# Optimization experiments

Hardware: AMD Instinct MI355X
Metric: run time of the kernel (lower is better)

Reference implementation:

```python
import jax, jax.numpy as jnp
import numpy as np

B, T, V, E, H = 256, 512, 30000, 256, 32


def _run_dir(x, mask, Wih, Whh, bih, bhh, reverse):
    # x: [B,T,D], mask: [B,T] bool. PyTorch GRU gate order: r, z, n.
    gi = jnp.einsum('btd,gd->btg', x, Wih) + bih  # precompute input gates [B,T,3H]
    h0 = jnp.zeros((x.shape[0], Whh.shape[1]), x.dtype)

    def step(h, inp):
        gi_t, m_t = inp
        gh = h @ Whh.T + bhh
        ir, iz, inn = jnp.split(gi_t, 3, axis=-1)
        hr, hz, hn = jnp.split(gh, 3, axis=-1)
        r = jax.nn.sigmoid(ir + hr)
        z = jax.nn.sigmoid(iz + hz)
        n = jnp.tanh(inn + r * hn)
        h_new = (1.0 - z) * n + z * h
        # packed-sequence semantics: freeze state at padded steps
        h = jnp.where(m_t[:, None], h_new, h)
        return h, h

    hT, ys = jax.lax.scan(step, h0, (jnp.swapaxes(gi, 0, 1), mask.T), reverse=reverse)
    return jnp.swapaxes(ys, 0, 1), hT  # outputs [B,T,H], final hidden [B,H]


def _bigru_layer(x, mask, pf, pb):
    of, hf = _run_dir(x, mask, *pf, reverse=False)
    ob, hb = _run_dir(x, mask, *pb, reverse=True)
    return jnp.concatenate([of, ob], axis=-1), hf, hb


def setup_inputs() -> dict:
    key = jax.random.key(0)
    ks = jax.random.split(key, 24)
    lengths = jax.random.randint(ks[0], (B,), 1, T + 1)
    mask = (jnp.arange(T)[None, :] < lengths[:, None]).astype(jnp.int32)
    ids = jax.random.randint(ks[1], (B, T), 1, V)
    ids = jnp.where(mask > 0, ids, 0)  # pad_id = 0 at padded positions
    embed = (jax.random.normal(ks[2], (V, E), jnp.float32) * 0.1).at[0].set(0.0)

    def gru_params(k, din):
        k1, k2, k3, k4 = jax.random.split(k, 4)
        s = 1.0 / np.sqrt(H)
        return (jax.random.uniform(k1, (3 * H, din), jnp.float32, -s, s),
                jax.random.uniform(k2, (3 * H, H), jnp.float32, -s, s),
                jax.random.uniform(k3, (3 * H,), jnp.float32, -s, s),
                jax.random.uniform(k4, (3 * H,), jnp.float32, -s, s))

    inp = {"input_ids": ids, "attention_mask": mask, "embed": embed}
    i = 3
    for layer, din in (("l0", E), ("l1", 2 * H)):
        for d in ("f", "b"):
            Wih, Whh, bih, bhh = gru_params(ks[i], din); i += 1
            inp[f"Wih_{layer}{d}"] = Wih
            inp[f"Whh_{layer}{d}"] = Whh
            inp[f"bih_{layer}{d}"] = bih
            inp[f"bhh_{layer}{d}"] = bhh
    s = 1.0 / np.sqrt(2 * H)
    inp["Wout"] = jax.random.uniform(ks[i], (6, 2 * H), jnp.float32, -s, s)
    inp["bout"] = jax.random.uniform(ks[i + 1], (6,), jnp.float32, -s, s)
    return inp


def reference(input_ids, attention_mask, embed,
              Wih_l0f, Whh_l0f, bih_l0f, bhh_l0f,
              Wih_l0b, Whh_l0b, bih_l0b, bhh_l0b,
              Wih_l1f, Whh_l1f, bih_l1f, bhh_l1f,
              Wih_l1b, Whh_l1b, bih_l1b, bhh_l1b,
              Wout, bout):
    mask = attention_mask > 0
    x = embed[input_ids]  # [B,T,E]
    x1, _, _ = _bigru_layer(x, mask,
                            (Wih_l0f, Whh_l0f, bih_l0f, bhh_l0f),
                            (Wih_l0b, Whh_l0b, bih_l0b, bhh_l0b))
    # no dropout: eval-mode forward
    _, hf, hb = _bigru_layer(x1, mask,
                             (Wih_l1f, Whh_l1f, bih_l1f, bhh_l1f),
                             (Wih_l1b, Whh_l1b, bih_l1b, bhh_l1b))
    top = jnp.concatenate([hf, hb], axis=-1)  # h_n[-2:] -> [B, 2H]
    return top @ Wout.T + bout  # [B, 6]
```

## Files before the change

kernel.cpp:

```cpp
#include <hip/hip_runtime.h>
#include <hip/hip_bf16.h>
#include <stdint.h>

#define B_ 256
#define T_ 512
#define V_ 30000
#define E_ 256
#define H_ 32

typedef float v2f __attribute__((ext_vector_type(2)));

__device__ __forceinline__ float sigmoidf_fast(float x) {
    return 1.0f / (1.0f + __expf(-x));
}
__device__ __forceinline__ float tanhf_fast(float x) {
    return 1.0f - 2.0f / (1.0f + __expf(2.0f * x));
}
__device__ __forceinline__ uint32_t rlu(float v, int lane) {
    return (uint32_t)__builtin_amdgcn_readlane(__float_as_int(v), lane);
}
__device__ __forceinline__ void pk_fma(v2f& acc, v2f w, uint64_t hh) {
    asm("v_pk_fma_f32 %0, %1, %2, %0" : "+v"(acc) : "v"(w), "s"(hh));
}

#define GEMM_MT 64
#define GEMM_KC 32
#define GEMM_PA 68
#define GEMM_PB 196

__global__ __launch_bounds__(256) void gemm_gates(
    const float* __restrict__ A, int M, int K,
    const float* __restrict__ Wf, const float* __restrict__ Wb,
    const float* __restrict__ bihf, const float* __restrict__ bhhf,
    const float* __restrict__ bihb, const float* __restrict__ bhhb,
    float* __restrict__ Out)
{
    __shared__ float As[GEMM_KC][GEMM_PA];
    __shared__ float Bs[GEMM_KC][GEMM_PB];

    const int tid = threadIdx.x;
    const int mbase = blockIdx.x * GEMM_MT;
    const int mg = tid >> 5, ng = tid & 31;
    const int m_off = mg * 8, n_off = ng * 6;

    float acc[8][6];
    #pragma unroll
    for (int r = 0; r < 8; ++r)
        #pragma unroll
        for (int c = 0; c < 6; ++c) acc[r][c] = 0.f;

    for (int kc = 0; kc < K; kc += GEMM_KC) {
        #pragma unroll
        for (int i = 0; i < 2; ++i) {
            int fi = tid + 256 * i;
            int row = fi >> 3, cf = fi & 7;
            int m = mbase + row;
            float4 v = make_float4(0.f, 0.f, 0.f, 0.f);
            if (m < M) v = *(const float4*)&A[(size_t)m * K + kc + cf * 4];
            As[cf * 4 + 0][row] = v.x; As[cf * 4 + 1][row] = v.y;
            As[cf * 4 + 2][row] = v.z; As[cf * 4 + 3][row] = v.w;
        }
        #pragma unroll
        for (int i = 0; i < 6; ++i) {
            int fi = tid + 256 * i;
            int g = fi >> 3, cf = fi & 7;
            const float* Wsel = (g < 96) ? (Wf + (size_t)g * K)
                                         : (Wb + (size_t)(g - 96) * K);
            float4 v = *(const float4*)&Wsel[kc + cf * 4];
            Bs[cf * 4 + 0][g] = v.x; Bs[cf * 4 + 1][g] = v.y;
            Bs[cf * 4 + 2][g] = v.z; Bs[cf * 4 + 3][g] = v.w;
        }
        __syncthreads();
        #pragma unroll
        for (int k = 0; k < GEMM_KC; ++k) {
            float a[8], bb[6];
            *(float4*)&a[0] = *(const float4*)&As[k][m_off];
            *(float4*)&a[4] = *(const float4*)&As[k][m_off + 4];
            *(float2*)&bb[0] = *(const float2*)&Bs[k][n_off];
            *(float2*)&bb[2] = *(const float2*)&Bs[k][n_off + 2];
            *(float2*)&bb[4] = *(const float2*)&Bs[k][n_off + 4];
            #pragma unroll
            for (int r = 0; r < 8; ++r)
                #pragma unroll
                for (int c = 0; c < 6; ++c)
                    acc[r][c] = fmaf(a[r], bb[c], acc[r][c]);
        }
        __syncthreads();
    }

    float bias[6];
    #pragma unroll
    for (int c = 0; c < 6; ++c) {
        int g = n_off + c;
        int g96 = (g < 96) ? g : g - 96;
        const float* bih = (g < 96) ? bihf : bihb;
        const float* bhh = (g < 96) ? bhhf : bhhb;
        bias[c] = bih[g96] + ((g96 < 64) ? bhh[g96] : 0.f);
    }
    #pragma unroll
    for (int r = 0; r < 8; ++r) {
        int m = mbase + m_off + r;
        if (m < M) {
            float* op = &Out[(size_t)m * 192 + n_off];
            #pragma unroll
            for (int c = 0; c < 6; ++c) op[c] = acc[r][c] + bias[c];
        }
    }
}

template <int USE_IDS>
__global__ __launch_bounds__(64)
__attribute__((amdgpu_waves_per_eu(1, 1)))
void gru_scan(
    const float* __restrict__ gi,
    const int* __restrict__ ids,
    const int* __restrict__ mask,
    const float* __restrict__ Whh_f, const float* __restrict__ Whh_b,
    const float* __restrict__ bhh_f, const float* __restrict__ bhh_b,
    float* __restrict__ out_seq,
    float* __restrict__ out_fin)
{
    const int l = threadIdx.x;
    const int j = l & 31;
    const bool lower = l < 32;
    const int dir = blockIdx.x & 1;
    const int b = blockIdx.x >> 1;
    const int bT = b * T_;

    const float* Whh = dir ? Whh_b : Whh_f;
    const float* bhh = dir ? bhh_b : bhh_f;

    v2f wR[16], wZ[16], wN[16];
    #pragma unroll
    for (int q = 0; q < 16; ++q) {
        wR[q] = *(const v2f*)&Whh[j * 32 + 2 * q];
        wZ[q] = *(const v2f*)&Whh[(32 + j) * 32 + 2 * q];
        wN[q] = *(const v2f*)&Whh[(64 + j) * 32 + 2 * q];
    }
    const float bn = bhh[64 + j];

    const int offR = dir * 96 + j;
    const int offZ = dir * 96 + 32 + j;
    const int offN = dir * 96 + 64 + j;

    auto wbase = [&](int c) { return dir ? (bT + 508 - 4 * c) : (bT + 4 * c); };

    int4 ids0 = make_int4(0, 0, 0, 0);
    if (USE_IDS) ids0 = *(const int4*)&ids[wbase(0)];
    int4 mask_use = *(const int4*)&mask[wbase(0)];
    int4 mask_mid = *(const int4*)&mask[wbase(1)];
    int4 mask_in  = make_int4(0, 0, 0, 0);
    int4 ids_pf = make_int4(0, 0, 0, 0), ids_mid = ids_pf, ids_in = ids_pf;
    if (USE_IDS) {
        ids_pf  = *(const int4*)&ids[wbase(1)];
        ids_mid = *(const int4*)&ids[wbase(2)];
    }

    float gR[2][4], gZ[2][4], gN[2][4];
    #pragma unroll
    for (int u = 0; u < 4; ++u) {
        int row;
        if (USE_IDS) {
            const int* ip = (const int*)&ids0;
            row = dir ? ip[3 - u] : ip[u];
        } else {
            row = bT + (dir ? (511 - u) : u);
        }
        const float* gp = gi + (size_t)row * 192;
        gR[0][u] = gp[offR];
        gZ[0][u] = gp[offZ];
        gN[0][u] = gp[offN];
    }

    float h = 0.f;

    for (int c2 = 0; c2 < 64; ++c2) {
        #pragma unroll
        for (int p = 0; p < 2; ++p) {
            const int c = 2 * c2 + p;
            if (USE_IDS) {
                const int ci = (c + 3 < 128) ? (c + 3) : 127;
                ids_in = *(const int4*)&ids[wbase(ci)];
            }
            {
                const int cm = (c + 2 < 128) ? (c + 2) : 127;
                mask_in = *(const int4*)&mask[wbase(cm)];
            }
            const int cN = (c + 1 < 128) ? (c + 1) : 127;

            #pragma unroll
            for (int u = 0; u < 4; ++u) {
                int rowN;
                if (USE_IDS) {
                    const int* ip = (const int*)&ids_pf;
                    rowN = dir ? ip[3 - u] : ip[u];
                } else {
                    rowN = bT + (dir ? (511 - 4 * cN - u) : (4 * cN + u));
                }
                const float* gpN = gi + (size_t)rowN * 192;
                gR[p ^ 1][u] = gpN[offR];
                gZ[p ^ 1][u] = gpN[offZ];
                gN[p ^ 1][u] = gpN[offN];

                const int* mu = (const int*)&mask_use;
                const int m = dir ? mu[3 - u] : mu[u];

                v2f aR = {0.f, 0.f}, aZ = {0.f, 0.f}, aN = {0.f, 0.f};
                #pragma unroll
                for (int k = 0; k < 16; ++k) {
                    const uint32_t hlo = rlu(h, 2 * k);
                    const uint32_t hhi = rlu(h, 2 * k + 1);
                    const uint64_t hh = ((uint64_t)hhi << 32) | hlo;
                    pk_fma(aR, wR[k], hh);
                    pk_fma(aZ, wZ[k], hh);
                    pk_fma(aN, wN[k], hh);
                }
                const float r  = sigmoidf_fast(gR[p][u] + aR.x + aR.y);
                const float z  = sigmoidf_fast(gZ[p][u] + aZ.x + aZ.y);
                const float hn = bn + aN.x + aN.y;
                const float n  = tanhf_fast(gN[p][u] + r * hn);
                const float hnew = n + z * (h - n);
                h = m ? hnew : h;

                if (out_seq != nullptr) {
                    const int t = dir ? (511 - 4 * c - u) : (4 * c + u);
                    if (lower)
                        out_seq[(size_t)(bT + t) * 64 + dir * 32 + j] = h;
                }
            }
            mask_use = mask_mid; mask_mid = mask_in;
            if (USE_IDS) { ids_pf = ids_mid; ids_mid = ids_in; }
        }
    }

    if (out_fin != nullptr && lower)
        out_fin[b * 64 + dir * 32 + j] = h;
}

__global__ void head_kernel(const float* __restrict__ hfin,
                            const float* __restrict__ Wout,
                            const float* __restrict__ bout,
                            float* __restrict__ out)
{
    int idx = blockIdx.x * blockDim.x + threadIdx.x;
    if (idx >= B_ * 6) return;
    int b = idx / 6, o = idx % 6;
    float acc = bout[o];
    const float* hp = hfin + b * 64;
    const float* wp = Wout + o * 64;
    #pragma unroll
    for (int k = 0; k < 64; ++k) acc = fmaf(hp[k], wp[k], acc);
    out[idx] = acc;
}

extern "C" void kernel_launch(void* const* d_in, const int* in_sizes, int n_in,
                              void* d_out, int out_size, void* d_ws, size_t ws_size,
                              hipStream_t stream)
{
    const int*   ids   = (const int*)d_in[0];
    const int*   mask  = (const int*)d_in[1];
    const float* embed = (const float*)d_in[2];
    const float* Wih0f = (const float*)d_in[3];
    const float* Whh0f = (const float*)d_in[4];
    const float* bih0f = (const float*)d_in[5];
    const float* bhh0f = (const float*)d_in[6];
    const float* Wih0b = (const float*)d_in[7];
    const float* Whh0b = (const float*)d_in[8];
    const float* bih0b = (const float*)d_in[9];
    const float* bhh0b = (const float*)d_in[10];
    const float* Wih1f = (const float*)d_in[11];
    const float* Whh1f = (const float*)d_in[12];
    const float* bih1f = (const float*)d_in[13];
    const float* bhh1f = (const float*)d_in[14];
    const float* Wih1b = (const float*)d_in[15];
    const float* Whh1b = (const float*)d_in[16];
    const float* bih1b = (const float*)d_in[17];
    const float* bhh1b = (const float*)d_in[18];
    const float* Wout  = (const float*)d_in[19];
    const float* bout  = (const float*)d_in[20];

    float* ws   = (float*)d_ws;
    float* gbuf = ws;
    float* x1   = ws + (size_t)B_ * T_ * 192;
    float* hfin = x1 + (size_t)B_ * T_ * 64;

    gemm_gates<<<(V_ + GEMM_MT - 1) / GEMM_MT, 256, 0, stream>>>(
        embed, V_, E_, Wih0f, Wih0b, bih0f, bhh0f, bih0b, bhh0b, gbuf);

    gru_scan<1><<<2 * B_, 64, 0, stream>>>(
        gbuf, ids, mask, Whh0f, Whh0b, bhh0f, bhh0b, x1, nullptr);

    gemm_gates<<<(B_ * T_) / GEMM_MT, 256, 0, stream>>>(
        x1, B_ * T_, 64, Wih1f, Wih1b, bih1f, bhh1f, bih1b, bhh1b, gbuf);

    gru_scan<0><<<2 * B_, 64, 0, stream>>>(
        gbuf, nullptr, mask, Whh1f, Whh1b, bhh1f, bhh1b, nullptr, hfin);

    head_kernel<<<(B_ * 6 + 255) / 256, 256, 0, stream>>>(hfin, Wout, bout,
                                                          (float*)d_out);
}
```

Measured before the change: 568.9 us.

## Pack both GRU directions into one wave using ds_swizzle broadcast

```diff
diff --git a/kernel.cpp b/kernel.cpp
--- a/kernel.cpp
+++ b/kernel.cpp
@@ -8,19 +8,11 @@
 #define E_ 256
 #define H_ 32
 
-typedef float v2f __attribute__((ext_vector_type(2)));
-
 __device__ __forceinline__ float sigmoidf_fast(float x) {
     return 1.0f / (1.0f + __expf(-x));
 }
 __device__ __forceinline__ float tanhf_fast(float x) {
     return 1.0f - 2.0f / (1.0f + __expf(2.0f * x));
-}
-__device__ __forceinline__ uint32_t rlu(float v, int lane) {
-    return (uint32_t)__builtin_amdgcn_readlane(__float_as_int(v), lane);
-}
-__device__ __forceinline__ void pk_fma(v2f& acc, v2f w, uint64_t hh) {
-    asm("v_pk_fma_f32 %0, %1, %2, %0" : "+v"(acc) : "v"(w), "s"(hh));
 }
 
 #define GEMM_MT 64
@@ -107,6 +99,23 @@
         }
     }
 }
+
+#define MV_STEP(K) {                                                          \
+    const float hk = __int_as_float(                                         \
+        __builtin_amdgcn_ds_swizzle(__float_as_int(h), ((K) << 5)));          \
+    aR[(K) & 3] = fmaf(wR[K], hk, aR[(K) & 3]);                               \
+    aZ[(K) & 3] = fmaf(wZ[K], hk, aZ[(K) & 3]);                               \
+    aN[(K) & 3] = fmaf(wN[K], hk, aN[(K) & 3]); }
+
+#define MV_ALL()                                                              \
+    MV_STEP(0)  MV_STEP(1)  MV_STEP(2)  MV_STEP(3)                            \
+    MV_STEP(4)  MV_STEP(5)  MV_STEP(6)  MV_STEP(7)                            \
+    MV_STEP(8)  MV_STEP(9)  MV_STEP(10) MV_STEP(11)                           \
+    MV_STEP(12) MV_STEP(13) MV_STEP(14) MV_STEP(15)                           \
+    MV_STEP(16) MV_STEP(17) MV_STEP(18) MV_STEP(19)                           \
+    MV_STEP(20) MV_STEP(21) MV_STEP(22) MV_STEP(23)                           \
+    MV_STEP(24) MV_STEP(25) MV_STEP(26) MV_STEP(27)                           \
+    MV_STEP(28) MV_STEP(29) MV_STEP(30) MV_STEP(31)
 
 template <int USE_IDS>
 __global__ __launch_bounds__(64)
@@ -122,20 +131,25 @@
 {
     const int l = threadIdx.x;
     const int j = l & 31;
-    const bool lower = l < 32;
-    const int dir = blockIdx.x & 1;
-    const int b = blockIdx.x >> 1;
+    const int dir = l >> 5;
+    const int b = blockIdx.x;
     const int bT = b * T_;
 
     const float* Whh = dir ? Whh_b : Whh_f;
     const float* bhh = dir ? bhh_b : bhh_f;
 
-    v2f wR[16], wZ[16], wN[16];
-    #pragma unroll
-    for (int q = 0; q < 16; ++q) {
-        wR[q] = *(const v2f*)&Whh[j * 32 + 2 * q];
-        wZ[q] = *(const v2f*)&Whh[(32 + j) * 32 + 2 * q];
-        wN[q] = *(const v2f*)&Whh[(64 + j) * 32 + 2 * q];
+    float wR[32], wZ[32], wN[32];
+    #pragma unroll
+    for (int q = 0; q < 8; ++q) {
+        float4 a = *(const float4*)&Whh[j * 32 + q * 4];
+        wR[q * 4 + 0] = a.x; wR[q * 4 + 1] = a.y;
+        wR[q * 4 + 2] = a.z; wR[q * 4 + 3] = a.w;
+        float4 zq = *(const float4*)&Whh[(32 + j) * 32 + q * 4];
+        wZ[q * 4 + 0] = zq.x; wZ[q * 4 + 1] = zq.y;
+        wZ[q * 4 + 2] = zq.z; wZ[q * 4 + 3] = zq.w;
+        float4 nq = *(const float4*)&Whh[(64 + j) * 32 + q * 4];
+        wN[q * 4 + 0] = nq.x; wN[q * 4 + 1] = nq.y;
+        wN[q * 4 + 2] = nq.z; wN[q * 4 + 3] = nq.w;
     }
     const float bn = bhh[64 + j];
 
@@ -205,27 +219,24 @@
                 const int* mu = (const int*)&mask_use;
                 const int m = dir ? mu[3 - u] : mu[u];
 
-                v2f aR = {0.f, 0.f}, aZ = {0.f, 0.f}, aN = {0.f, 0.f};
-                #pragma unroll
-                for (int k = 0; k < 16; ++k) {
-                    const uint32_t hlo = rlu(h, 2 * k);
-                    const uint32_t hhi = rlu(h, 2 * k + 1);
-                    const uint64_t hh = ((uint64_t)hhi << 32) | hlo;
-                    pk_fma(aR, wR[k], hh);
-                    pk_fma(aZ, wZ[k], hh);
-                    pk_fma(aN, wN[k], hh);
-                }
-                const float r  = sigmoidf_fast(gR[p][u] + aR.x + aR.y);
-                const float z  = sigmoidf_fast(gZ[p][u] + aZ.x + aZ.y);
-                const float hn = bn + aN.x + aN.y;
+                float aR[4] = {0.f, 0.f, 0.f, 0.f};
+                float aZ[4] = {0.f, 0.f, 0.f, 0.f};
+                float aN[4] = {0.f, 0.f, 0.f, 0.f};
+                MV_ALL();
+                const float dR = (aR[0] + aR[1]) + (aR[2] + aR[3]);
+                const float dZ = (aZ[0] + aZ[1]) + (aZ[2] + aZ[3]);
+                const float dN = (aN[0] + aN[1]) + (aN[2] + aN[3]);
+
+                const float r  = sigmoidf_fast(gR[p][u] + dR);
+                const float z  = sigmoidf_fast(gZ[p][u] + dZ);
+                const float hn = bn + dN;
                 const float n  = tanhf_fast(gN[p][u] + r * hn);
                 const float hnew = n + z * (h - n);
                 h = m ? hnew : h;
 
                 if (out_seq != nullptr) {
                     const int t = dir ? (511 - 4 * c - u) : (4 * c + u);
-                    if (lower)
-                        out_seq[(size_t)(bT + t) * 64 + dir * 32 + j] = h;
+                    out_seq[(size_t)(bT + t) * 64 + dir * 32 + j] = h;
                 }
             }
             mask_use = mask_mid; mask_mid = mask_in;
@@ -233,7 +244,7 @@
         }
     }
 
-    if (out_fin != nullptr && lower)
+    if (out_fin != nullptr)
         out_fin[b * 64 + dir * 32 + j] = h;
 }
 
@@ -287,13 +298,13 @@
     gemm_gates<<<(V_ + GEMM_MT - 1) / GEMM_MT, 256, 0, stream>>>(
         embed, V_, E_, Wih0f, Wih0b, bih0f, bhh0f, bih0b, bhh0b, gbuf);
 
-    gru_scan<1><<<2 * B_, 64, 0, stream>>>(
+    gru_scan<1><<<B_, 64, 0, stream>>>(
         gbuf, ids, mask, Whh0f, Whh0b, bhh0f, bhh0b, x1, nullptr);
 
     gemm_gates<<<(B_ * T_) / GEMM_MT, 256, 0, stream>>>(
         x1, B_ * T_, 64, Wih1f, Wih1b, bih1f, bhh1f, bih1b, bhh1b, gbuf);
 
-    gru_scan<0><<<2 * B_, 64, 0, stream>>>(
+    gru_scan<0><<<B_, 64, 0, stream>>>(
         gbuf, nullptr, mask, Whh1f, Whh1b, bhh1f, bhh1b, nullptr, hfin);
 
     head_kernel<<<(B_ * 6 + 255) / 256, 256, 0, stream>>>(hfin, Wout, bout,
```

After: 859.3 us. 1.51x slower.
